# Optimization experiments

Measured on AMD Instinct MI355X. Metric: run time of the kernel, lower is better.

The kernel has to match this reference:

```python
import jax, jax.numpy as jnp
import numpy as np

N, E, F, EF, T, C = 50000, 500000, 8, 4, 12, 32


def setup_inputs() -> dict:
    key = jax.random.key(0)
    ks = jax.random.split(key, 16)
    g = lambda i, shape, s=0.2: jax.random.normal(ks[i], shape, jnp.float32) * s
    return {
        "x": jax.random.normal(ks[0], (N, F, T), jnp.float32),
        "edge_index": jax.random.randint(ks[1], (2, E), 0, N),
        "edge_features": jax.random.normal(ks[2], (E, EF), jnp.float32),
        # feature_linear (F -> F)
        "feat_W": g(3, (F, F)), "feat_b": jnp.zeros((F,), jnp.float32),
        # edge_features_linear (EF -> 1)
        "ef_W": g(4, (EF, 1)), "ef_b": jnp.zeros((1,), jnp.float32),
        # A3TGCN attention over periods
        "attention": jax.random.uniform(ks[5], (T,), jnp.float32),
        # TGCN GCNConv weights (F -> C), bias included (PyG default)
        "conv_z_W": g(6, (F, C)), "conv_z_b": jnp.zeros((C,), jnp.float32),
        "conv_r_W": g(7, (F, C)), "conv_r_b": jnp.zeros((C,), jnp.float32),
        "conv_h_W": g(8, (F, C)), "conv_h_b": jnp.zeros((C,), jnp.float32),
        # TGCN gate linears (2C -> C)
        "lin_z_W": g(9, (2 * C, C)), "lin_z_b": jnp.zeros((C,), jnp.float32),
        "lin_r_W": g(10, (2 * C, C)), "lin_r_b": jnp.zeros((C,), jnp.float32),
        "lin_h_W": g(11, (2 * C, C)), "lin_h_b": jnp.zeros((C,), jnp.float32),
        # output head (C -> T)
        "head_W": g(12, (C, T)), "head_b": jnp.zeros((T,), jnp.float32),
    }


def _gcn_norm(edge_index, edge_weight, num_nodes):
    """PyG gcn_norm with add_self_loops=True (fill 1), flow source_to_target."""
    loops = jnp.arange(num_nodes)
    row = jnp.concatenate([edge_index[0], loops])  # sources
    col = jnp.concatenate([edge_index[1], loops])  # targets
    w = jnp.concatenate([edge_weight, jnp.ones((num_nodes,), edge_weight.dtype)])
    deg = jax.ops.segment_sum(w, col, num_segments=num_nodes)
    dinv = jnp.where(deg > 0, jax.lax.rsqrt(jnp.maximum(deg, 1e-12)), 0.0)
    norm = dinv[row] * w * dinv[col]
    return row, col, norm


def _forward(x, edge_index, edge_features, feat_W, feat_b, ef_W, ef_b,
             attention, conv_z_W, conv_z_b, conv_r_W, conv_r_b, conv_h_W,
             conv_h_b, lin_z_W, lin_z_b, lin_r_W, lin_r_b, lin_h_W, lin_h_b,
             head_W, head_b):
    num_nodes = x.shape[0]
    # feature linear over F: [N,F,T] -> [T,N,F]
    xt = jnp.transpose(x, (2, 0, 1)) @ feat_W + feat_b  # [T,N,F]
    # edge weight MLP: [E,EF] -> [E], relu
    ew = jax.nn.relu((edge_features @ ef_W + ef_b)[:, 0])
    row, col, norm = _gcn_norm(edge_index, ew, num_nodes)

    def gcn(h, W, b):
        msg = (h @ W)[row] * norm[:, None]  # [E+N, C]
        return jax.ops.segment_sum(msg, col, num_segments=num_nodes) + b

    def tgcn_cell(x_t):
        # A3TGCN passes H=None each period -> H starts at zeros every period
        H = jnp.zeros((num_nodes, C), x_t.dtype)
        Z = jax.nn.sigmoid(
            jnp.concatenate([gcn(x_t, conv_z_W, conv_z_b), H], 1) @ lin_z_W + lin_z_b)
        R = jax.nn.sigmoid(
            jnp.concatenate([gcn(x_t, conv_r_W, conv_r_b), H], 1) @ lin_r_W + lin_r_b)
        H_tilde = jnp.tanh(
            jnp.concatenate([gcn(x_t, conv_h_W, conv_h_b), H * R], 1) @ lin_h_W + lin_h_b)
        return Z * H + (1.0 - Z) * H_tilde

    probs = jax.nn.softmax(attention)

    def step(acc, inputs):
        x_t, p = inputs
        return acc + p * tgcn_cell(x_t), None

    H_accum, _ = jax.lax.scan(step, jnp.zeros((num_nodes, C), x.dtype), (xt, probs))
    h = jax.nn.relu(H_accum)
    return h @ head_W + head_b  # [N, T]


def reference(x, edge_index, edge_features, feat_W, feat_b, ef_W, ef_b,
              attention, conv_z_W, conv_z_b, conv_r_W, conv_r_b, conv_h_W,
              conv_h_b, lin_z_W, lin_z_b, lin_r_W, lin_r_b, lin_h_W, lin_h_b,
              head_W, head_b):
    return _forward(x, edge_index, edge_features, feat_W, feat_b, ef_W, ef_b,
                    attention, conv_z_W, conv_z_b, conv_r_W, conv_r_b,
                    conv_h_W, conv_h_b, lin_z_W, lin_z_b, lin_r_W, lin_r_b,
                    lin_h_W, lin_h_b, head_W, head_b)
```

## Files before the change

### kernel.cpp

```cpp
#include <hip/hip_runtime.h>
#include <math.h>

#define NN 50000
#define NE 500000
#define FD 8
#define EFD 4
#define TD 12
#define CD 32
#define FT (FD*TD)
#define SLOTS 48
#define ZB 49
#define ZV4 25000

__global__ __launch_bounds__(512) void kInit(
    float4* __restrict__ zp,
    const float* __restrict__ feat_W, const float* __restrict__ feat_b,
    const float* __restrict__ attention,
    const float* __restrict__ conv_z_W, const float* __restrict__ conv_z_b,
    const float* __restrict__ conv_h_W, const float* __restrict__ conv_h_b,
    const float* __restrict__ lin_z_W, const float* __restrict__ lin_z_b,
    const float* __restrict__ lin_h_W, const float* __restrict__ lin_h_b,
    float* __restrict__ consts)
{
    int tid = threadIdx.x;
    if (blockIdx.x < ZB) {
        int i = blockIdx.x * 512 + tid;
        if (i < ZV4) zp[i] = make_float4(0.f, 0.f, 0.f, 0.f);
        return;
    }
    __shared__ float WL[2][FD*CD];
    int half = tid >> 8;
    int idx  = tid & 255;
    int f = idx >> 5, c = idx & 31;
    const float* convW = half ? conv_h_W : conv_z_W;
    const float* linW  = half ? lin_h_W  : lin_z_W;
    float acc = 0.f;
    #pragma unroll
    for (int k = 0; k < CD; ++k)
        acc += convW[f*CD + k] * linW[k*CD + c];
    WL[half][idx] = acc;
    __syncthreads();
    float m = 0.f;
    #pragma unroll
    for (int g = 0; g < FD; ++g)
        m += feat_W[f*FD + g] * WL[half][g*CD + c];
    consts[half*256 + idx] = m;
    if (f == 0) {
        float a = 0.f;
        #pragma unroll
        for (int g = 0; g < FD; ++g)
            a += feat_b[g] * WL[half][g*CD + c];
        consts[512 + half*32 + c] = a;
        const float* convB = half ? conv_h_b : conv_z_b;
        const float* linB  = half ? lin_h_b : lin_z_b;
        float cc = linB[c];
        #pragma unroll
        for (int k = 0; k < CD; ++k)
            cc += convB[k] * linW[k*CD + c];
        consts[576 + half*32 + c] = cc;
    }
    if (tid == 0) {
        float mx = attention[0];
        for (int t = 1; t < TD; ++t) mx = fmaxf(mx, attention[t]);
        float e[TD], sum = 0.f;
        for (int t = 0; t < TD; ++t) { e[t] = expf(attention[t] - mx); sum += e[t]; }
        for (int t = 0; t < TD; ++t) consts[640 + t] = e[t] / sum;
    }
}

__global__ void kB1(const int* __restrict__ ei, const float* __restrict__ ef,
                    const float* __restrict__ ef_W, const float* __restrict__ ef_b,
                    unsigned long long* __restrict__ dc, int2* __restrict__ ep)
{
    int e = blockIdx.x * blockDim.x + threadIdx.x;
    if (e >= NE) return;
    float4 f4 = ((const float4*)ef)[e];
    float w = ef_b[0] + f4.x*ef_W[0] + f4.y*ef_W[1] + f4.z*ef_W[2] + f4.w*ef_W[3];
    if (w <= 0.f) return;
    int r = ei[e], c = ei[NE + e];
    unsigned long long pack = (1ULL << 56)
        | (unsigned long long)(w * 4294967296.0f);
    unsigned long long old = atomicAdd(&dc[c], pack);
    int pos = (int)(old >> 56);
    if (pos < SLOTS) ep[c * SLOTS + pos] = make_int2(r, __float_as_int(w));
}

__global__ void kDinv(const unsigned long long* __restrict__ dc,
                      float* __restrict__ dinv, int* __restrict__ cnt)
{
    int n = blockIdx.x * blockDim.x + threadIdx.x;
    if (n >= NN) return;
    unsigned long long v = dc[n];
    float deg = (float)(v & ((1ULL << 56) - 1)) * (1.0f / 4294967296.0f);
    dinv[n] = rsqrtf(deg + 1.0f);
    cnt[n] = (int)(v >> 56);
}

__global__ __launch_bounds__(256) void kGE(
    const float* __restrict__ x, const float* __restrict__ dinv,
    const int* __restrict__ cnt, const int2* __restrict__ ep,
    const float* __restrict__ consts, const float* __restrict__ head_W,
    const float* __restrict__ head_b, float* __restrict__ out)
{
    __shared__ float Mz[FD*CD], Mh[FD*CD];
    __shared__ float az[CD], ah[CD], cz[CD], ch[CD], p[TD];
    __shared__ float headW[CD*TD];
    __shared__ float ylds[8*FT];
    __shared__ float hlds[8*33];
    __shared__ float slds[8];
    int tid = threadIdx.x;
    Mz[tid] = consts[tid];
    Mh[tid] = consts[256 + tid];
    if (tid < CD) {
        az[tid] = consts[512 + tid]; ah[tid] = consts[544 + tid];
        cz[tid] = consts[576 + tid]; ch[tid] = consts[608 + tid];
    }
    if (tid < TD) p[tid] = consts[640 + tid];
    headW[tid] = head_W[tid];
    if (tid < CD*TD - 256) headW[256 + tid] = head_W[256 + tid];
    int base = blockIdx.x * 8;

    if (tid < 192) {
        int ln = tid / 24, g = tid - ln * 24;
        int n = base + ln;
        const float4* x4 = (const float4*)x;
        float di = dinv[n];
        float d2 = di * di;
        float4 xv = x4[(size_t)n * 24 + g];
        float4 acc;
        acc.x = d2*xv.x; acc.y = d2*xv.y; acc.z = d2*xv.z; acc.w = d2*xv.w;
        float sv = d2;
        int m = cnt[n];
        int st = n * SLOTS;
        if (m > 0) {
            int2 q[8];
            #pragma unroll
            for (int i = 0; i < 8; ++i) q[i] = ep[st + (i < m ? i : 0)];
            float dv[8];
            #pragma unroll
            for (int i = 0; i < 8; ++i) dv[i] = dinv[q[i].x];
            float4 xa[8];
            #pragma unroll
            for (int i = 0; i < 8; ++i) xa[i] = x4[(size_t)q[i].x * 24 + g];
            #pragma unroll
            for (int i = 0; i < 8; ++i) {
                float v = (i < m) ? __int_as_float(q[i].y) * dv[i] * di : 0.f;
                acc.x += v*xa[i].x; acc.y += v*xa[i].y;
                acc.z += v*xa[i].z; acc.w += v*xa[i].w;
                sv += v;
            }
            for (int j = st + 8, en = st + m; j < en; ++j) {
                int2 p0 = ep[j];
                float v0 = __int_as_float(p0.y) * dinv[p0.x] * di;
                float4 a0 = x4[(size_t)p0.x * 24 + g];
                acc.x += v0*a0.x; acc.y += v0*a0.y;
                acc.z += v0*a0.z; acc.w += v0*a0.w;
                sv += v0;
            }
        }
        ((float4*)ylds)[tid] = acc;
        if (g == 0) slds[ln] = sv;
    }
    __syncthreads();

    int g = tid >> 5, c = tid & 31;
    const float* yn = ylds + g * FT;
    float sn = slds[g];
    float bz = cz[c] + sn * az[c];
    float bh = ch[c] + sn * ah[c];
    float pz[TD], ph[TD];
    #pragma unroll
    for (int t = 0; t < TD; ++t) { pz[t] = bz; ph[t] = bh; }
    #pragma unroll
    for (int f = 0; f < FD; ++f) {
        float mzv = Mz[f*CD + c], mhv = Mh[f*CD + c];
        float yv[TD];
        *(float4*)&yv[0] = *(const float4*)(yn + f*TD + 0);
        *(float4*)&yv[4] = *(const float4*)(yn + f*TD + 4);
        *(float4*)&yv[8] = *(const float4*)(yn + f*TD + 8);
        #pragma unroll
        for (int t = 0; t < TD; ++t) {
            pz[t] += yv[t] * mzv;
            ph[t] += yv[t] * mhv;
        }
    }
    float acc = 0.f;
    #pragma unroll
    for (int t = 0; t < TD; ++t) {
        float omz = __builtin_amdgcn_rcpf(1.f + __expf(pz[t]));
        float th  = 1.f - 2.f * __builtin_amdgcn_rcpf(1.f + __expf(2.f*ph[t]));
        acc += p[t] * omz * th;
    }
    hlds[g*33 + c] = fmaxf(acc, 0.f);
    __syncthreads();

    if (tid < 8*TD) {
        int n0 = tid / TD, tt = tid - n0*TD;
        float v = head_b[tt];
        const float* hn = hlds + n0*33;
        #pragma unroll
        for (int cc = 0; cc < CD; ++cc) v += hn[cc] * headW[cc*TD + tt];
        out[(size_t)(base + n0)*TD + tt] = v;
    }
}

extern "C" void kernel_launch(void* const* d_in, const int* in_sizes, int n_in,
                              void* d_out, int out_size, void* d_ws, size_t ws_size,
                              hipStream_t stream)
{
    const float* x      = (const float*)d_in[0];
    const int*   ei     = (const int*)  d_in[1];
    const float* ef     = (const float*)d_in[2];
    const float* feat_W = (const float*)d_in[3];
    const float* feat_b = (const float*)d_in[4];
    const float* ef_W   = (const float*)d_in[5];
    const float* ef_b   = (const float*)d_in[6];
    const float* att    = (const float*)d_in[7];
    const float* czW    = (const float*)d_in[8];
    const float* czb    = (const float*)d_in[9];
    const float* chW    = (const float*)d_in[12];
    const float* chb    = (const float*)d_in[13];
    const float* lzW    = (const float*)d_in[14];
    const float* lzb    = (const float*)d_in[15];
    const float* lhW    = (const float*)d_in[18];
    const float* lhb    = (const float*)d_in[19];
    const float* hW     = (const float*)d_in[20];
    const float* hb     = (const float*)d_in[21];
    float* out = (float*)d_out;

    unsigned long long* dc   = (unsigned long long*)d_ws;
    float*              dinv = (float*)(dc + NN);
    int*                cnt  = (int*)(dinv + NN);
    float*              cst  = (float*)(cnt + NN);
    int2*               ep   = (int2*)(cst + 1024);

    kInit<<<ZB + 1, 512, 0, stream>>>((float4*)dc, feat_W, feat_b, att,
                                      czW, czb, chW, chb, lzW, lzb, lhW, lhb, cst);
    kB1<<<(NE + 255)/256, 256, 0, stream>>>(ei, ef, ef_W, ef_b, dc, ep);
    kDinv<<<(NN + 255)/256, 256, 0, stream>>>(dc, dinv, cnt);
    kGE<<<NN/8, 256, 0, stream>>>(x, dinv, cnt, ep, cst, hW, hb, out);
}
```

Before: 62.21 us.

## Pad edge slots with zero-weight self entries, use packed FMA and register constants

kDinv now fills the unused first 8 edge slots of each node with a zero-weight entry pointing to the node itself. This lets kGE load 8 neighbours unconditionally, without the m>0 branch or per-slot select masks. The GCN-to-gate projection is rewritten with inline v_pk_fma_f32 on 2-wide vectors, and the per-channel constants are held in registers instead of LDS. Index math also drops the size_t casts. These changes add register pressure and extra stores in kDinv, and the int index math is only safe while the products fit in 32 bits.

```diff
diff --git a/kernel.cpp b/kernel.cpp
--- a/kernel.cpp
+++ b/kernel.cpp
@@ -11,6 +11,8 @@
 #define SLOTS 48
 #define ZB 49
 #define ZV4 25000
+
+typedef float f32x2 __attribute__((ext_vector_type(2)));
 
 __global__ __launch_bounds__(512) void kInit(
     float4* __restrict__ zp,
@@ -86,14 +88,18 @@
 }
 
 __global__ void kDinv(const unsigned long long* __restrict__ dc,
-                      float* __restrict__ dinv, int* __restrict__ cnt)
+                      float* __restrict__ dinv, int* __restrict__ cnt,
+                      int2* __restrict__ ep)
 {
     int n = blockIdx.x * blockDim.x + threadIdx.x;
     if (n >= NN) return;
     unsigned long long v = dc[n];
     float deg = (float)(v & ((1ULL << 56) - 1)) * (1.0f / 4294967296.0f);
     dinv[n] = rsqrtf(deg + 1.0f);
-    cnt[n] = (int)(v >> 56);
+    int m = (int)(v >> 56);
+    cnt[n] = m;
+    int2 pad = make_int2(n, 0);
+    for (int i = m; i < 8; ++i) ep[n * SLOTS + i] = pad;
 }
 
 __global__ __launch_bounds__(256) void kGE(
@@ -102,20 +108,23 @@
     const float* __restrict__ consts, const float* __restrict__ head_W,
     const float* __restrict__ head_b, float* __restrict__ out)
 {
-    __shared__ float Mz[FD*CD], Mh[FD*CD];
-    __shared__ float az[CD], ah[CD], cz[CD], ch[CD], p[TD];
     __shared__ float headW[CD*TD];
     __shared__ float ylds[8*FT];
     __shared__ float hlds[8*33];
     __shared__ float slds[8];
     int tid = threadIdx.x;
-    Mz[tid] = consts[tid];
-    Mh[tid] = consts[256 + tid];
-    if (tid < CD) {
-        az[tid] = consts[512 + tid]; ah[tid] = consts[544 + tid];
-        cz[tid] = consts[576 + tid]; ch[tid] = consts[608 + tid];
-    }
-    if (tid < TD) p[tid] = consts[640 + tid];
+    int c0 = tid & 31;
+    float mzr[FD], mhr[FD];
+    #pragma unroll
+    for (int f = 0; f < FD; ++f) {
+        mzr[f] = consts[f*CD + c0];
+        mhr[f] = consts[256 + f*CD + c0];
+    }
+    float azc = consts[512 + c0], ahc = consts[544 + c0];
+    float czc = consts[576 + c0], chc = consts[608 + c0];
+    float pt[TD];
+    #pragma unroll
+    for (int t = 0; t < TD; ++t) pt[t] = consts[640 + t];
     headW[tid] = head_W[tid];
     if (tid < CD*TD - 256) headW[256 + tid] = head_W[256 + tid];
     int base = blockIdx.x * 8;
@@ -126,72 +135,83 @@
         const float4* x4 = (const float4*)x;
         float di = dinv[n];
         float d2 = di * di;
-        float4 xv = x4[(size_t)n * 24 + g];
+        float4 xv = x4[n * 24 + g];
         float4 acc;
         acc.x = d2*xv.x; acc.y = d2*xv.y; acc.z = d2*xv.z; acc.w = d2*xv.w;
         float sv = d2;
         int m = cnt[n];
         int st = n * SLOTS;
-        if (m > 0) {
-            int2 q[8];
-            #pragma unroll
-            for (int i = 0; i < 8; ++i) q[i] = ep[st + (i < m ? i : 0)];
-            float dv[8];
-            #pragma unroll
-            for (int i = 0; i < 8; ++i) dv[i] = dinv[q[i].x];
-            float4 xa[8];
-            #pragma unroll
-            for (int i = 0; i < 8; ++i) xa[i] = x4[(size_t)q[i].x * 24 + g];
-            #pragma unroll
-            for (int i = 0; i < 8; ++i) {
-                float v = (i < m) ? __int_as_float(q[i].y) * dv[i] * di : 0.f;
-                acc.x += v*xa[i].x; acc.y += v*xa[i].y;
-                acc.z += v*xa[i].z; acc.w += v*xa[i].w;
-                sv += v;
-            }
-            for (int j = st + 8, en = st + m; j < en; ++j) {
-                int2 p0 = ep[j];
-                float v0 = __int_as_float(p0.y) * dinv[p0.x] * di;
-                float4 a0 = x4[(size_t)p0.x * 24 + g];
-                acc.x += v0*a0.x; acc.y += v0*a0.y;
-                acc.z += v0*a0.z; acc.w += v0*a0.w;
-                sv += v0;
-            }
+        int2 q[8];
+        #pragma unroll
+        for (int i = 0; i < 8; ++i) q[i] = ep[st + i];
+        float dv[8];
+        #pragma unroll
+        for (int i = 0; i < 8; ++i) dv[i] = dinv[q[i].x];
+        float4 xa[8];
+        #pragma unroll
+        for (int i = 0; i < 8; ++i) xa[i] = x4[q[i].x * 24 + g];
+        #pragma unroll
+        for (int i = 0; i < 8; ++i) {
+            float v = __int_as_float(q[i].y) * dv[i] * di;
+            acc.x += v*xa[i].x; acc.y += v*xa[i].y;
+            acc.z += v*xa[i].z; acc.w += v*xa[i].w;
+            sv += v;
+        }
+        for (int j = st + 8, en = st + m; j < en; ++j) {
+            int2 p0 = ep[j];
+            float v0 = __int_as_float(p0.y) * dinv[p0.x] * di;
+            float4 a0 = x4[p0.x * 24 + g];
+            acc.x += v0*a0.x; acc.y += v0*a0.y;
+            acc.z += v0*a0.z; acc.w += v0*a0.w;
+            sv += v0;
         }
         ((float4*)ylds)[tid] = acc;
         if (g == 0) slds[ln] = sv;
     }
     __syncthreads();
 
-    int g = tid >> 5, c = tid & 31;
-    const float* yn = ylds + g * FT;
+    int g = tid >> 5;
+    const float4* yf4 = (const float4*)(ylds + g * FT);
     float sn = slds[g];
-    float bz = cz[c] + sn * az[c];
-    float bh = ch[c] + sn * ah[c];
-    float pz[TD], ph[TD];
-    #pragma unroll
-    for (int t = 0; t < TD; ++t) { pz[t] = bz; ph[t] = bh; }
+    float bz = czc + sn * azc;
+    float bh = chc + sn * ahc;
+    f32x2 pz2[6], ph2[6];
+    #pragma unroll
+    for (int k = 0; k < 6; ++k) {
+        pz2[k].x = bz; pz2[k].y = bz;
+        ph2[k].x = bh; ph2[k].y = bh;
+    }
     #pragma unroll
     for (int f = 0; f < FD; ++f) {
-        float mzv = Mz[f*CD + c], mhv = Mh[f*CD + c];
-        float yv[TD];
-        *(float4*)&yv[0] = *(const float4*)(yn + f*TD + 0);
-        *(float4*)&yv[4] = *(const float4*)(yn + f*TD + 4);
-        *(float4*)&yv[8] = *(const float4*)(yn + f*TD + 8);
-        #pragma unroll
-        for (int t = 0; t < TD; ++t) {
-            pz[t] += yv[t] * mzv;
-            ph[t] += yv[t] * mhv;
+        float4 ya = yf4[f*3 + 0], yb = yf4[f*3 + 1], yc = yf4[f*3 + 2];
+        f32x2 y2[6];
+        y2[0].x = ya.x; y2[0].y = ya.y;  y2[1].x = ya.z; y2[1].y = ya.w;
+        y2[2].x = yb.x; y2[2].y = yb.y;  y2[3].x = yb.z; y2[3].y = yb.w;
+        y2[4].x = yc.x; y2[4].y = yc.y;  y2[5].x = yc.z; y2[5].y = yc.w;
+        f32x2 mz2, mh2;
+        mz2.x = mzr[f]; mz2.y = mzr[f];
+        mh2.x = mhr[f]; mh2.y = mhr[f];
+        #pragma unroll
+        for (int k = 0; k < 6; ++k) {
+            asm volatile("v_pk_fma_f32 %0, %1, %2, %0"
+                         : "+v"(pz2[k]) : "v"(y2[k]), "v"(mz2));
+            asm volatile("v_pk_fma_f32 %0, %1, %2, %0"
+                         : "+v"(ph2[k]) : "v"(y2[k]), "v"(mh2));
         }
     }
     float acc = 0.f;
     #pragma unroll
-    for (int t = 0; t < TD; ++t) {
-        float omz = __builtin_amdgcn_rcpf(1.f + __expf(pz[t]));
-        float th  = 1.f - 2.f * __builtin_amdgcn_rcpf(1.f + __expf(2.f*ph[t]));
-        acc += p[t] * omz * th;
-    }
-    hlds[g*33 + c] = fmaxf(acc, 0.f);
+    for (int k = 0; k < 6; ++k) {
+        #pragma unroll
+        for (int h = 0; h < 2; ++h) {
+            float pzv = (h == 0) ? pz2[k].x : pz2[k].y;
+            float phv = (h == 0) ? ph2[k].x : ph2[k].y;
+            float omz = __builtin_amdgcn_rcpf(1.f + __expf(pzv));
+            float th  = 1.f - 2.f * __builtin_amdgcn_rcpf(1.f + __expf(2.f*phv));
+            acc += pt[2*k + h] * omz * th;
+        }
+    }
+    hlds[g*33 + c0] = fmaxf(acc, 0.f);
     __syncthreads();
 
     if (tid < 8*TD) {
@@ -237,6 +257,6 @@
     kInit<<<ZB + 1, 512, 0, stream>>>((float4*)dc, feat_W, feat_b, att,
                                       czW, czb, chW, chb, lzW, lzb, lhW, lhb, cst);
     kB1<<<(NE + 255)/256, 256, 0, stream>>>(ei, ef, ef_W, ef_b, dc, ep);
-    kDinv<<<(NN + 255)/256, 256, 0, stream>>>(dc, dinv, cnt);
+    kDinv<<<(NN + 255)/256, 256, 0, stream>>>(dc, dinv, cnt, ep);
     kGE<<<NN/8, 256, 0, stream>>>(x, dinv, cnt, ep, cst, hW, hb, out);
 }
```

Result: faster. 60.65 us (-2.5%).
